# Optimization experiments

Measured on AMD Instinct MI355X. Metric: run time of the kernel, lower is better.

## Reference

```python
import jax, jax.numpy as jnp
import numpy as np

FEATURE_DIM = 512
HIDDEN_DIM = 512
N_HEADS = 8
HEAD_DIM = HIDDEN_DIM // N_HEADS
MAX_LEN = 5000
GAMMA = 0.5  # gaussian relative-position bias width
LN_EPS = 1e-5


def make_pe(d_model, max_len):
    # sinusoidal positional encoding buffer, as in PositionalEncoding.__init__
    pos = jnp.arange(max_len, dtype=jnp.float32)[:, None]
    div = jnp.exp(jnp.arange(0, d_model, 2, dtype=jnp.float32) * (-np.log(10000.0) / d_model))
    ang = pos * div  # [max_len, d_model/2]
    pe = jnp.zeros((max_len, d_model), dtype=jnp.float32)
    pe = pe.at[:, 0::2].set(jnp.sin(ang)).at[:, 1::2].set(jnp.cos(ang))
    return pe


def setup_inputs() -> dict:
    key = jax.random.key(0)
    k_x, k_q, k_k, k_v = jax.random.split(key, 4)
    xavier = np.sqrt(6.0 / (FEATURE_DIM + HEAD_DIM))  # xavier_uniform over last two dims
    return {
        "data_window": jax.random.normal(k_x, (1, 2048, FEATURE_DIM), dtype=jnp.float32),
        "W_query": jax.random.uniform(k_q, (N_HEADS, FEATURE_DIM, HEAD_DIM), jnp.float32, -xavier, xavier),
        "W_key": jax.random.uniform(k_k, (N_HEADS, FEATURE_DIM, HEAD_DIM), jnp.float32, -xavier, xavier),
        "W_value": jax.random.uniform(k_v, (N_HEADS, FEATURE_DIM, HEAD_DIM), jnp.float32, -xavier, xavier),
        "ln_gamma": jnp.ones((FEATURE_DIM,), dtype=jnp.float32),
        "ln_beta": jnp.zeros((FEATURE_DIM,), dtype=jnp.float32),
    }


def reference(data_window, W_query, W_key, W_value, ln_gamma, ln_beta):
    B, S, F = data_window.shape
    temperature = 1.0

    # LayerNorm over feature dim
    mu = jnp.mean(data_window, axis=-1, keepdims=True)
    var = jnp.mean(jnp.square(data_window - mu), axis=-1, keepdims=True)
    x = (data_window - mu) * jax.lax.rsqrt(var + LN_EPS) * ln_gamma + ln_beta

    # positional encoding, exactly as original: x + pe[:x.shape[0]] (requires B==1)
    pe = make_pe(FEATURE_DIM, MAX_LEN)
    x = x + pe[:B]  # [B,F] broadcasts over [B,S,F] only because B==1

    # per-head QKV projections, vectorized over heads
    Q = jnp.einsum('bsf,hfd->bhsd', x, W_query)
    K = jnp.einsum('bsf,hfd->bhsd', x, W_key)
    V = jnp.einsum('bsf,hfd->bhsd', x, W_value)

    scores = jnp.einsum('bhsd,bhtd->bhst', Q, K) / np.sqrt(HEAD_DIM)

    # gaussian relative-position bias: scale(=1) * exp(-gamma * (i-j)^2)
    p = jnp.arange(S, dtype=jnp.float32)
    rel = p[:, None] - p[None, :]
    bias = jnp.exp(-GAMMA * jnp.square(rel))  # [S,S]
    scores = (scores + bias[None, None]) / temperature
    # dropout on scores is identity in eval mode

    attn = jax.nn.softmax(scores, axis=-1)  # [B,H,S,S]
    head_out = jnp.einsum('bhst,bhtd->bhsd', attn, V)

    # concat heads along feature dim: [B,S,H*D]
    multi_head_output = head_out.transpose(0, 2, 1, 3).reshape(B, S, N_HEADS * HEAD_DIM)
    mean_weights = jnp.mean(attn, axis=1)  # [B,S,S]
    return multi_head_output, mean_weights
```

## Files before the change

### kernel.cpp

```cpp
#include <hip/hip_runtime.h>
#include <hip/hip_bf16.h>
#include <math.h>

#define S_LEN 2048
#define FDIM  512
#define NH    8
#define HD    64
#define MH_ELEMS (S_LEN * FDIM)
#define MEAN_ELEMS (S_LEN * S_LEN)
#define LOG2E 1.44269504f
#define LN2   0.69314718f

typedef _Float16 half_t;
typedef _Float16 half2v __attribute__((ext_vector_type(2)));
typedef _Float16 half4v __attribute__((ext_vector_type(4)));
typedef _Float16 half8v __attribute__((ext_vector_type(8)));
typedef float    float4v __attribute__((ext_vector_type(4)));
typedef int      int4v   __attribute__((ext_vector_type(4)));

#define MFMA16(a, b, c) __builtin_amdgcn_mfma_f32_16x16x32_f16((a), (b), (c), 0, 0, 0)

static __device__ __forceinline__ float fast_exp2(float x) {
    return __builtin_amdgcn_exp2f(x);
}

__global__ __launch_bounds__(256) void prep_kernel(const float* __restrict__ x,
                                                   const float* __restrict__ gamma,
                                                   const float* __restrict__ beta,
                                                   const float* __restrict__ Wq,
                                                   const float* __restrict__ Wk,
                                                   const float* __restrict__ Wv,
                                                   half_t* __restrict__ xo,
                                                   half_t* __restrict__ WT) {
    const int tid = threadIdx.x;
    if (blockIdx.x < 2048) {
        const int row = blockIdx.x;
        const float2 v = ((const float2*)(x + (size_t)row * FDIM))[tid];
        float s = v.x + v.y;
        float q = v.x * v.x + v.y * v.y;
        #pragma unroll
        for (int off = 1; off < 64; off <<= 1) {
            s += __shfl_xor(s, off, 64);
            q += __shfl_xor(q, off, 64);
        }
        __shared__ float red[8];
        const int wave = tid >> 6;
        if ((tid & 63) == 0) { red[wave] = s; red[4 + wave] = q; }
        __syncthreads();
        s = red[0] + red[1] + red[2] + red[3];
        q = red[4] + red[5] + red[6] + red[7];
        const float mu  = s * (1.0f / FDIM);
        const float var = q * (1.0f / FDIM) - mu * mu;
        const float rstd = rsqrtf(var + 1e-5f);
        const int f0 = tid * 2, f1 = tid * 2 + 1;
        const float o0 = (v.x - mu) * rstd * gamma[f0] + beta[f0];
        const float o1 = (v.y - mu) * rstd * gamma[f1] + beta[f1] + 1.0f;
        half2v o; o.x = (half_t)o0; o.y = (half_t)o1;
        ((half2v*)(xo + (size_t)row * FDIM))[tid] = o;
    } else {
        const int idx = blockIdx.x - 2048;
        const int k0 = (idx & 7) * 64;
        const int h  = (idx >> 3) & 7;
        const int z  = idx >> 6;
        const float* W = ((z == 0) ? Wq : (z == 1) ? Wk : Wv) + (size_t)h * FDIM * HD;
        __shared__ float Ls[64][65];
        {
            const int kk = tid >> 2, dg = (tid & 3) * 16;
            #pragma unroll
            for (int j = 0; j < 4; ++j) {
                const float4 w = *(const float4*)(W + (size_t)(k0 + kk) * HD + dg + j * 4);
                Ls[kk][dg + j * 4 + 0] = w.x; Ls[kk][dg + j * 4 + 1] = w.y;
                Ls[kk][dg + j * 4 + 2] = w.z; Ls[kk][dg + j * 4 + 3] = w.w;
            }
        }
        __syncthreads();
        {
            const int d = tid >> 2, kg = (tid & 3) * 16;
            half8v t0, t1;
            #pragma unroll
            for (int j = 0; j < 8; ++j) t0[j] = (half_t)Ls[kg + j][d];
            #pragma unroll
            for (int j = 0; j < 8; ++j) t1[j] = (half_t)Ls[kg + 8 + j][d];
            half_t* dst = WT + ((size_t)(z * NH + h) * HD + d) * FDIM + k0 + kg;
            *(half8v*)dst = t0;
            *(half8v*)(dst + 8) = t1;
        }
    }
}

__global__ __launch_bounds__(256) void qkv_kernel(const half_t* __restrict__ xh,
                                                  const half_t* __restrict__ WT,
                                                  half_t* __restrict__ Qo,
                                                  half_t* __restrict__ Ko,
                                                  half_t* __restrict__ VTo) {
    const int ms0 = blockIdx.x * 128;
    const int h   = blockIdx.y, z = blockIdx.z;
    const half_t* Wt = WT + (size_t)(z * NH + h) * HD * FDIM;

    const int tid = threadIdx.x;
    const int wv = tid >> 6, lane = tid & 63;
    const int lo = lane & 15, qq = lane >> 4;

    float4v acc[2][4];
    #pragma unroll
    for (int rg = 0; rg < 2; ++rg)
        #pragma unroll
        for (int cg = 0; cg < 4; ++cg) acc[rg][cg] = (float4v){0.f, 0.f, 0.f, 0.f};

    const half_t* ar[2];
    ar[0] = xh + (size_t)(ms0 + wv * 32 + lo) * FDIM + qq * 8;
    ar[1] = ar[0] + 16 * FDIM;
    const half_t* wrow[4];
    #pragma unroll
    for (int cg = 0; cg < 4; ++cg) wrow[cg] = Wt + (size_t)(cg * 16 + lo) * FDIM + qq * 8;

    half8v a_c[2][2], b_c[4][2];
    #pragma unroll
    for (int rg = 0; rg < 2; ++rg) { a_c[rg][0] = *(const half8v*)(ar[rg]); a_c[rg][1] = *(const half8v*)(ar[rg] + 32); }
    #pragma unroll
    for (int cg = 0; cg < 4; ++cg) { b_c[cg][0] = *(const half8v*)(wrow[cg]); b_c[cg][1] = *(const half8v*)(wrow[cg] + 32); }

    for (int k0 = 0; k0 < FDIM; k0 += 64) {
        const int kn0 = (k0 + 64 < FDIM) ? k0 + 64 : 0;
        const int kn1 = (k0 + 96 < FDIM) ? k0 + 96 : 0;
        half8v a_n[2][2], b_n[4][2];
        #pragma unroll
        for (int rg = 0; rg < 2; ++rg) { a_n[rg][0] = *(const half8v*)(ar[rg] + kn0); a_n[rg][1] = *(const half8v*)(ar[rg] + kn1); }
        #pragma unroll
        for (int cg = 0; cg < 4; ++cg) { b_n[cg][0] = *(const half8v*)(wrow[cg] + kn0); b_n[cg][1] = *(const half8v*)(wrow[cg] + kn1); }
        #pragma unroll
        for (int kh = 0; kh < 2; ++kh)
            #pragma unroll
            for (int rg = 0; rg < 2; ++rg)
                #pragma unroll
                for (int cg = 0; cg < 4; ++cg)
                    acc[rg][cg] = MFMA16(a_c[rg][kh], b_c[cg][kh], acc[rg][cg]);
        #pragma unroll
        for (int rg = 0; rg < 2; ++rg) { a_c[rg][0] = a_n[rg][0]; a_c[rg][1] = a_n[rg][1]; }
        #pragma unroll
        for (int cg = 0; cg < 4; ++cg) { b_c[cg][0] = b_n[cg][0]; b_c[cg][1] = b_n[cg][1]; }
    }

    if (z < 2) {
        half_t* Co = ((z == 0) ? Qo : Ko) + (size_t)h * S_LEN * HD;
        #pragma unroll
        for (int rg = 0; rg < 2; ++rg)
            #pragma unroll
            for (int cg = 0; cg < 4; ++cg)
                #pragma unroll
                for (int r = 0; r < 4; ++r)
                    Co[(size_t)(ms0 + wv * 32 + rg * 16 + qq * 4 + r) * HD + cg * 16 + lo] =
                        (half_t)acc[rg][cg][r];
    } else {
        __shared__ float Ls[128][65];
        #pragma unroll
        for (int rg = 0; rg < 2; ++rg)
            #pragma unroll
            for (int cg = 0; cg < 4; ++cg)
                #pragma unroll
                for (int r = 0; r < 4; ++r)
                    Ls[wv * 32 + rg * 16 + qq * 4 + r][cg * 16 + lo] = acc[rg][cg][r];
        __syncthreads();
        const int d = tid & 63, sg = tid >> 6;
        half_t* dst = VTo + (size_t)(h * HD + d) * S_LEN + ms0 + sg * 32;
        #pragma unroll
        for (int c = 0; c < 4; ++c) {
            half8v t;
            #pragma unroll
            for (int j = 0; j < 8; ++j) t[j] = (half_t)Ls[sg * 32 + c * 8 + j][d];
            *(half8v*)(dst + c * 8) = t;
        }
    }
}

__global__ __launch_bounds__(256) void attn2_kernel(const half_t* __restrict__ Qw,
                                                    const half_t* __restrict__ Kw,
                                                    const half_t* __restrict__ VT,
                                                    half_t* __restrict__ Op,
                                                    float* __restrict__ mp,
                                                    float* __restrict__ lp) {
    const int s0 = blockIdx.x * 32;
    const int h  = blockIdx.y;
    const int z  = blockIdx.z;
    const half_t* Qh = Qw + (size_t)h * S_LEN * HD;
    const half_t* Kh = Kw + (size_t)h * S_LEN * HD;
    const half_t* Vt = VT + (size_t)h * (size_t)HD * S_LEN;

    __shared__ float Osh[4][32][65];
    __shared__ float lsh[4][32];
    __shared__ float msh[4][32];

    const int tid = threadIdx.x;
    const int wv = tid >> 6, lane = tid & 63;
    const int lo = lane & 15, qq = lane >> 4;
    const int tb = z * 1024 + wv * 256;

    const half8v qA0 = *(const half8v*)(Qh + (size_t)(s0 + lo) * HD + qq * 8);
    const half8v qA1 = *(const half8v*)(Qh + (size_t)(s0 + lo) * HD + 32 + qq * 8);
    const half8v qB0 = *(const half8v*)(Qh + (size_t)(s0 + 16 + lo) * HD + qq * 8);
    const half8v qB1 = *(const half8v*)(Qh + (size_t)(s0 + 16 + lo) * HD + 32 + qq * 8);

    float4v accA[4], accB[4];
    #pragma unroll
    for (int dt = 0; dt < 4; ++dt) {
        accA[dt] = (float4v){0.f, 0.f, 0.f, 0.f};
        accB[dt] = (float4v){0.f, 0.f, 0.f, 0.f};
    }
    float mA = 0.f, mB = 0.f, lA = 0.f, lB = 0.f;

    const int srcLow  = lo + ((qq & 1) * 2) * 16;
    const int srcHigh = srcLow + 16;
    const bool sel1 = (qq >> 1) != 0;

    half8v kc[4];
    {
        const half_t* kp0 = Kh + (size_t)(tb + lo) * HD;
        const half_t* kp1 = Kh + (size_t)(tb + 16 + lo) * HD;
        kc[0] = *(const half8v*)(kp0 + qq * 8);
        kc[1] = *(const half8v*)(kp0 + 32 + qq * 8);
        kc[2] = *(const half8v*)(kp1 + qq * 8);
        kc[3] = *(const half8v*)(kp1 + 32 + qq * 8);
    }

    for (int ps = 0; ps < 8; ++ps) {
        const int Tg  = tb + ps * 32;
        const int Tgn = tb + ((ps < 7) ? ps + 1 : ps) * 32;
        half8v kn[4], vc[4];
        {
            const half_t* kp0 = Kh + (size_t)(Tgn + lo) * HD;
            const half_t* kp1 = Kh + (size_t)(Tgn + 16 + lo) * HD;
            kn[0] = *(const half8v*)(kp0 + qq * 8);
            kn[1] = *(const half8v*)(kp0 + 32 + qq * 8);
            kn[2] = *(const half8v*)(kp1 + qq * 8);
            kn[3] = *(const half8v*)(kp1 + 32 + qq * 8);
            #pragma unroll
            for (int dt = 0; dt < 4; ++dt)
                vc[dt] = *(const half8v*)(Vt + (size_t)(dt * 16 + lo) * S_LEN + Tg + qq * 8);
        }
        float4v c0A = (float4v){0.f, 0.f, 0.f, 0.f};
        c0A = MFMA16(kc[0], qA0, c0A); c0A = MFMA16(kc[1], qA1, c0A);
        float4v c1A = (float4v){0.f, 0.f, 0.f, 0.f};
        c1A = MFMA16(kc[2], qA0, c1A); c1A = MFMA16(kc[3], qA1, c1A);
        float4v c0B = (float4v){0.f, 0.f, 0.f, 0.f};
        c0B = MFMA16(kc[0], qB0, c0B); c0B = MFMA16(kc[1], qB1, c0B);
        float4v c1B = (float4v){0.f, 0.f, 0.f, 0.f};
        c1B = MFMA16(kc[2], qB0, c1B); c1B = MFMA16(kc[3], qB1, c1B);

        const int dd0 = s0 - Tg;
        const bool nA0 = (dd0 > -40) && (dd0 < 40);
        const bool nA1 = (dd0 - 16 > -40) && (dd0 - 16 < 40);
        const bool nB0 = (dd0 + 16 > -40) && (dd0 + 16 < 40);
        const bool nB1 = nA0;
        float S0A[4], S1A[4], S0B[4], S1B[4];
        #pragma unroll
        for (int r = 0; r < 4; ++r) {
            const int t0 = Tg + qq * 4 + r, t1 = t0 + 16;
            float sa0 = c0A[r] * 0.125f;
            if (nA0) { const float d = (float)(s0 + lo - t0); sa0 += __expf(-0.5f * d * d); }
            float sa1 = c1A[r] * 0.125f;
            if (nA1) { const float d = (float)(s0 + lo - t1); sa1 += __expf(-0.5f * d * d); }
            float sb0 = c0B[r] * 0.125f;
            if (nB0) { const float d = (float)(s0 + 16 + lo - t0); sb0 += __expf(-0.5f * d * d); }
            float sb1 = c1B[r] * 0.125f;
            if (nB1) { const float d = (float)(s0 + 16 + lo - t1); sb1 += __expf(-0.5f * d * d); }
            S0A[r] = sa0 * LOG2E; S1A[r] = sa1 * LOG2E;
            S0B[r] = sb0 * LOG2E; S1B[r] = sb1 * LOG2E;
        }
        float smA = fmaxf(fmaxf(fmaxf(S0A[0], S0A[1]), fmaxf(S0A[2], S0A[3])),
                          fmaxf(fmaxf(S1A[0], S1A[1]), fmaxf(S1A[2], S1A[3])));
        float smB = fmaxf(fmaxf(fmaxf(S0B[0], S0B[1]), fmaxf(S0B[2], S0B[3])),
                          fmaxf(fmaxf(S1B[0], S1B[1]), fmaxf(S1B[2], S1B[3])));
        smA = fmaxf(smA, __shfl_xor(smA, 16, 64));
        smA = fmaxf(smA, __shfl_xor(smA, 32, 64));
        smB = fmaxf(smB, __shfl_xor(smB, 16, 64));
        smB = fmaxf(smB, __shfl_xor(smB, 32, 64));
        const float gmax = fmaxf(smA - mA, smB - mB);
        if (!__all(gmax <= 5.77f)) {
            const float mnA = fmaxf(mA, smA), mnB = fmaxf(mB, smB);
            const float alA = fast_exp2(mA - mnA), alB = fast_exp2(mB - mnB);
            mA = mnA; mB = mnB;
            lA *= alA; lB *= alB;
            #pragma unroll
            for (int dt = 0; dt < 4; ++dt)
                #pragma unroll
                for (int i = 0; i < 4; ++i) { accA[dt][i] *= alA; accB[dt][i] *= alB; }
        }
        float E0A[4], E1A[4], E0B[4], E1B[4];
        float lsA = 0.f, lsB = 0.f;
        #pragma unroll
        for (int r = 0; r < 4; ++r) {
            E0A[r] = fast_exp2(S0A[r] - mA); E1A[r] = fast_exp2(S1A[r] - mA);
            E0B[r] = fast_exp2(S0B[r] - mB); E1B[r] = fast_exp2(S1B[r] - mB);
            lsA += E0A[r] + E1A[r];
            lsB += E0B[r] + E1B[r];
        }
        lA += lsA;
        lB += lsB;

        int pkA0, pkA1, pkA2, pkA3, pkB0, pkB1, pkB2, pkB3;
        {
            half2v p;
            p.x = (half_t)E0A[0]; p.y = (half_t)E0A[1]; pkA0 = __builtin_bit_cast(int, p);
            p.x = (half_t)E0A[2]; p.y = (half_t)E0A[3]; pkA1 = __builtin_bit_cast(int, p);
            p.x = (half_t)E1A[0]; p.y = (half_t)E1A[1]; pkA2 = __builtin_bit_cast(int, p);
            p.x = (half_t)E1A[2]; p.y = (half_t)E1A[3]; pkA3 = __builtin_bit_cast(int, p);
            p.x = (half_t)E0B[0]; p.y = (half_t)E0B[1]; pkB0 = __builtin_bit_cast(int, p);
            p.x = (half_t)E0B[2]; p.y = (half_t)E0B[3]; pkB1 = __builtin_bit_cast(int, p);
            p.x = (half_t)E1B[0]; p.y = (half_t)E1B[1]; pkB2 = __builtin_bit_cast(int, p);
            p.x = (half_t)E1B[2]; p.y = (half_t)E1B[3]; pkB3 = __builtin_bit_cast(int, p);
        }
        int4v biA, biB;
        {
            const int l0a = __shfl(pkA0, srcLow, 64),  l0b = __shfl(pkA2, srcLow, 64);
            const int l1a = __shfl(pkA1, srcLow, 64),  l1b = __shfl(pkA3, srcLow, 64);
            const int h0a = __shfl(pkA0, srcHigh, 64), h0b = __shfl(pkA2, srcHigh, 64);
            const int h1a = __shfl(pkA1, srcHigh, 64), h1b = __shfl(pkA3, srcHigh, 64);
            biA[0] = sel1 ? l0b : l0a;
            biA[1] = sel1 ? l1b : l1a;
            biA[2] = sel1 ? h0b : h0a;
            biA[3] = sel1 ? h1b : h1a;
        }
        {
            const int l0a = __shfl(pkB0, srcLow, 64),  l0b = __shfl(pkB2, srcLow, 64);
            const int l1a = __shfl(pkB1, srcLow, 64),  l1b = __shfl(pkB3, srcLow, 64);
            const int h0a = __shfl(pkB0, srcHigh, 64), h0b = __shfl(pkB2, srcHigh, 64);
            const int h1a = __shfl(pkB1, srcHigh, 64), h1b = __shfl(pkB3, srcHigh, 64);
            biB[0] = sel1 ? l0b : l0a;
            biB[1] = sel1 ? l1b : l1a;
            biB[2] = sel1 ? h0b : h0a;
            biB[3] = sel1 ? h1b : h1a;
        }
        const half8v bpA = __builtin_bit_cast(half8v, biA);
        const half8v bpB = __builtin_bit_cast(half8v, biB);
        #pragma unroll
        for (int dt = 0; dt < 4; ++dt) {
            accA[dt] = MFMA16(vc[dt], bpA, accA[dt]);
            accB[dt] = MFMA16(vc[dt], bpB, accB[dt]);
        }
        #pragma unroll
        for (int i = 0; i < 4; ++i) kc[i] = kn[i];
    }

    lA += __shfl_xor(lA, 16, 64); lA += __shfl_xor(lA, 32, 64);
    lB += __shfl_xor(lB, 16, 64); lB += __shfl_xor(lB, 32, 64);
    if (qq == 0) {
        lsh[wv][lo] = lA;      msh[wv][lo] = mA;
        lsh[wv][16 + lo] = lB; msh[wv][16 + lo] = mB;
    }
    #pragma unroll
    for (int dt = 0; dt < 4; ++dt)
        #pragma unroll
        for (int r = 0; r < 4; ++r) {
            Osh[wv][lo][dt * 16 + qq * 4 + r]      = accA[dt][r];
            Osh[wv][16 + lo][dt * 16 + qq * 4 + r] = accB[dt][r];
        }
    __syncthreads();

    #pragma unroll
    for (int p = 0; p < 2; ++p) {
        const int q = p * 16 + (tid >> 4), dg = tid & 15;
        const float m0 = msh[0][q], m1 = msh[1][q], m2 = msh[2][q], m3 = msh[3][q];
        const float M = fmaxf(fmaxf(m0, m1), fmaxf(m2, m3));
        const float f0 = fast_exp2(m0 - M), f1 = fast_exp2(m1 - M);
        const float f2 = fast_exp2(m2 - M), f3 = fast_exp2(m3 - M);
        const float L = lsh[0][q] * f0 + lsh[1][q] * f1 + lsh[2][q] * f2 + lsh[3][q] * f3;
        half4v o;
        #pragma unroll
        for (int i = 0; i < 4; ++i) {
            const float ov = Osh[0][q][dg * 4 + i] * f0 + Osh[1][q][dg * 4 + i] * f1 +
                             Osh[2][q][dg * 4 + i] * f2 + Osh[3][q][dg * 4 + i] * f3;
            o[i] = (half_t)ov;
        }
        const size_t pidx = (size_t)(z * NH + h) * S_LEN + s0 + q;
        *(half4v*)(Op + pidx * HD + dg * 4) = o;
        if (dg == 0) { mp[pidx] = M * LN2; lp[pidx] = L; }
    }
}

__global__ __launch_bounds__(256) void mean2_kernel(const half_t* __restrict__ Qw,
                                                    const half_t* __restrict__ Kw,
                                                    const half_t* __restrict__ Op,
                                                    const float* __restrict__ mp,
                                                    const float* __restrict__ lp,
                                                    float* __restrict__ out) {
    const int q0 = blockIdx.x * 32;
    const int tbase = blockIdx.y * 256;
    const int tid = threadIdx.x;

    __shared__ float lnc[NH][32];
    __shared__ float g0s[NH][32];
    __shared__ float g1s[NH][32];
    {
        const int h = tid >> 5, qi = tid & 31;
        const size_t i0 = (size_t)h * S_LEN + q0 + qi;
        const size_t i1 = (size_t)(NH + h) * S_LEN + q0 + qi;
        const float m0 = mp[i0], m1 = mp[i1];
        const float M = fmaxf(m0, m1);
        const float f0 = __expf(m0 - M), f1 = __expf(m1 - M);
        const float L = lp[i0] * f0 + lp[i1] * f1;
        const float inv = 1.0f / L;
        lnc[h][qi] = -M - __logf(L);
        g0s[h][qi] = f0 * inv;
        g1s[h][qi] = f1 * inv;
    }
    __syncthreads();

    const int wv = tid >> 6, lane = tid & 63;
    const int lo = lane & 15, qq = lane >> 4;
    const int t0 = tbase + wv * 64;

    float4v macc[2][4];
    #pragma unroll
    for (int rg = 0; rg < 2; ++rg)
        #pragma unroll
        for (int tg = 0; tg < 4; ++tg) macc[rg][tg] = (float4v){0.f, 0.f, 0.f, 0.f};

    const half_t* qp = Qw + (size_t)(q0 + lo) * HD + qq * 8;
    const half_t* kp = Kw + (size_t)(t0 + lo) * HD + qq * 8;

    #pragma unroll 2
    for (int h = 0; h < NH; ++h) {
        half8v a[2][2], b[4][2];
        #pragma unroll
        for (int rg = 0; rg < 2; ++rg) {
            a[rg][0] = *(const half8v*)(qp + (size_t)rg * 16 * HD);
            a[rg][1] = *(const half8v*)(qp + (size_t)rg * 16 * HD + 32);
        }
        #pragma unroll
        for (int tg = 0; tg < 4; ++tg) {
            b[tg][0] = *(const half8v*)(kp + (size_t)tg * 16 * HD);
            b[tg][1] = *(const half8v*)(kp + (size_t)tg * 16 * HD + 32);
        }
        float4v sacc[2][4];
        #pragma unroll
        for (int rg = 0; rg < 2; ++rg)
            #pragma unroll
            for (int tg = 0; tg < 4; ++tg) sacc[rg][tg] = (float4v){0.f, 0.f, 0.f, 0.f};
        #pragma unroll
        for (int kh = 0; kh < 2; ++kh)
            #pragma unroll
            for (int rg = 0; rg < 2; ++rg)
                #pragma unroll
                for (int tg = 0; tg < 4; ++tg)
                    sacc[rg][tg] = MFMA16(a[rg][kh], b[tg][kh], sacc[rg][tg]);

        const float4v ln0 = *(const float4v*)&lnc[h][qq * 4];
        const float4v ln1 = *(const float4v*)&lnc[h][16 + qq * 4];
        #pragma unroll
        for (int tg = 0; tg < 4; ++tg)
            #pragma unroll
            for (int r = 0; r < 4; ++r) {
                macc[0][tg][r] += __expf(fmaf(sacc[0][tg][r], 0.125f, ln0[r]));
                macc[1][tg][r] += __expf(fmaf(sacc[1][tg][r], 0.125f, ln1[r]));
            }
        qp += (size_t)S_LEN * HD;
        kp += (size_t)S_LEN * HD;
    }

    #pragma unroll
    for (int rg = 0; rg < 2; ++rg)
        #pragma unroll
        for (int tg = 0; tg < 4; ++tg) {
            const int tgl = t0 + tg * 16;
            const bool near = ((q0 + 31 - tgl) > -40) && ((q0 - (tgl + 15)) < 40);
            #pragma unroll
            for (int r = 0; r < 4; ++r) {
                const int qe = q0 + rg * 16 + qq * 4 + r;
                const int te = tgl + lo;
                float w = macc[rg][tg][r] * 0.125f;
                if (near) {
                    const float d = (float)(qe - te);
                    w *= __expf(__expf(-0.5f * d * d));
                }
                out[MH_ELEMS + (size_t)qe * S_LEN + te] = w;
            }
        }

    if (blockIdx.y == 0) {
        const int qi = tid >> 3, dg = (tid & 7) * 8;
        const int q = q0 + qi;
        #pragma unroll
        for (int h = 0; h < NH; ++h) {
            const half8v o0 = *(const half8v*)(Op + ((size_t)h * S_LEN + q) * HD + dg);
            const half8v o1 = *(const half8v*)(Op + ((size_t)(NH + h) * S_LEN + q) * HD + dg);
            const float a0 = g0s[h][qi], a1 = g1s[h][qi];
            float4 r0, r1;
            r0.x = (float)o0[0] * a0 + (float)o1[0] * a1;
            r0.y = (float)o0[1] * a0 + (float)o1[1] * a1;
            r0.z = (float)o0[2] * a0 + (float)o1[2] * a1;
            r0.w = (float)o0[3] * a0 + (float)o1[3] * a1;
            r1.x = (float)o0[4] * a0 + (float)o1[4] * a1;
            r1.y = (float)o0[5] * a0 + (float)o1[5] * a1;
            r1.z = (float)o0[6] * a0 + (float)o1[6] * a1;
            r1.w = (float)o0[7] * a0 + (float)o1[7] * a1;
            float* dst = out + (size_t)q * FDIM + h * HD + dg;
            *(float4*)dst = r0;
            *(float4*)(dst + 4) = r1;
        }
    }
}

extern "C" void kernel_launch(void* const* d_in, const int* in_sizes, int n_in,
                              void* d_out, int out_size, void* d_ws, size_t ws_size,
                              hipStream_t stream) {
    const float* x  = (const float*)d_in[0];
    const float* Wq = (const float*)d_in[1];
    const float* Wk = (const float*)d_in[2];
    const float* Wv = (const float*)d_in[3];
    const float* g  = (const float*)d_in[4];
    const float* b  = (const float*)d_in[5];
    float* out = (float*)d_out;
    char*  ws  = (char*)d_ws;

    half_t* Qh   = (half_t*)(ws);
    half_t* Kh   = (half_t*)(ws + (2ull  << 20));
    half_t* VT   = (half_t*)(ws + (4ull  << 20));
    half_t* xh   = (half_t*)(ws + (6ull  << 20));
    half_t* WT   = (half_t*)(ws + (8ull  << 20));
    half_t* Op   = (half_t*)(ws + (10ull << 20));
    float*  mp   = (float*) (ws + (14ull << 20));
    float*  lp   = (float*) (ws + (14ull << 20) + (128ull << 10));

    prep_kernel<<<2240, 256, 0, stream>>>(x, g, b, Wq, Wk, Wv, xh, WT);
    qkv_kernel<<<dim3(16, 8, 3), 256, 0, stream>>>(xh, WT, Qh, Kh, VT);
    attn2_kernel<<<dim3(64, 8, 2), 256, 0, stream>>>(Qh, Kh, VT, Op, mp, lp);
    mean2_kernel<<<dim3(64, 8), 256, 0, stream>>>(Qh, Kh, Op, mp, lp, out);
}
```

Before: 161.3 us.

## Shrink QKV tiles, prefetch per-head Q/K in mean kernel, simplify softmax rescaling

The QKV projection kernel now uses 64-row tiles with one row group per wave, doubling the grid to fill more CUs. The mean-weights kernel software-prefetches the next head's Q/K fragments while computing the current head and uses exp2 with a folded log2e scale. The attention kernel drops the lazy rescale threshold and the log2-domain scores, always rescaling accumulators with natural exp. Rescaling every tile adds ALU work in attention, while the other changes aim to hide load latency and improve occupancy.

```diff
diff --git a/kernel.cpp b/kernel.cpp
--- a/kernel.cpp
+++ b/kernel.cpp
@@ -9,7 +9,7 @@
 #define MH_ELEMS (S_LEN * FDIM)
 #define MEAN_ELEMS (S_LEN * S_LEN)
 #define LOG2E 1.44269504f
-#define LN2   0.69314718f
+#define QK_SCALE_L2 0.18033688f
 
 typedef _Float16 half_t;
 typedef _Float16 half2v __attribute__((ext_vector_type(2)));
@@ -93,7 +93,7 @@
                                                   half_t* __restrict__ Qo,
                                                   half_t* __restrict__ Ko,
                                                   half_t* __restrict__ VTo) {
-    const int ms0 = blockIdx.x * 128;
+    const int ms0 = blockIdx.x * 64;
     const int h   = blockIdx.y, z = blockIdx.z;
     const half_t* Wt = WT + (size_t)(z * NH + h) * HD * FDIM;
 
@@ -101,42 +101,33 @@
     const int wv = tid >> 6, lane = tid & 63;
     const int lo = lane & 15, qq = lane >> 4;
 
-    float4v acc[2][4];
-    #pragma unroll
-    for (int rg = 0; rg < 2; ++rg)
-        #pragma unroll
-        for (int cg = 0; cg < 4; ++cg) acc[rg][cg] = (float4v){0.f, 0.f, 0.f, 0.f};
-
-    const half_t* ar[2];
-    ar[0] = xh + (size_t)(ms0 + wv * 32 + lo) * FDIM + qq * 8;
-    ar[1] = ar[0] + 16 * FDIM;
+    float4v acc[4];
+    #pragma unroll
+    for (int cg = 0; cg < 4; ++cg) acc[cg] = (float4v){0.f, 0.f, 0.f, 0.f};
+
+    const half_t* ar = xh + (size_t)(ms0 + wv * 16 + lo) * FDIM + qq * 8;
     const half_t* wrow[4];
     #pragma unroll
     for (int cg = 0; cg < 4; ++cg) wrow[cg] = Wt + (size_t)(cg * 16 + lo) * FDIM + qq * 8;
 
-    half8v a_c[2][2], b_c[4][2];
-    #pragma unroll
-    for (int rg = 0; rg < 2; ++rg) { a_c[rg][0] = *(const half8v*)(ar[rg]); a_c[rg][1] = *(const half8v*)(ar[rg] + 32); }
+    half8v a_c[2], b_c[4][2];
+    a_c[0] = *(const half8v*)(ar); a_c[1] = *(const half8v*)(ar + 32);
     #pragma unroll
     for (int cg = 0; cg < 4; ++cg) { b_c[cg][0] = *(const half8v*)(wrow[cg]); b_c[cg][1] = *(const half8v*)(wrow[cg] + 32); }
 
     for (int k0 = 0; k0 < FDIM; k0 += 64) {
         const int kn0 = (k0 + 64 < FDIM) ? k0 + 64 : 0;
         const int kn1 = (k0 + 96 < FDIM) ? k0 + 96 : 0;
-        half8v a_n[2][2], b_n[4][2];
-        #pragma unroll
-        for (int rg = 0; rg < 2; ++rg) { a_n[rg][0] = *(const half8v*)(ar[rg] + kn0); a_n[rg][1] = *(const half8v*)(ar[rg] + kn1); }
+        half8v a_n[2], b_n[4][2];
+        a_n[0] = *(const half8v*)(ar + kn0); a_n[1] = *(const half8v*)(ar + kn1);
         #pragma unroll
         for (int cg = 0; cg < 4; ++cg) { b_n[cg][0] = *(const half8v*)(wrow[cg] + kn0); b_n[cg][1] = *(const half8v*)(wrow[cg] + kn1); }
         #pragma unroll
         for (int kh = 0; kh < 2; ++kh)
             #pragma unroll
-            for (int rg = 0; rg < 2; ++rg)
-                #pragma unroll
-                for (int cg = 0; cg < 4; ++cg)
-                    acc[rg][cg] = MFMA16(a_c[rg][kh], b_c[cg][kh], acc[rg][cg]);
-        #pragma unroll
-        for (int rg = 0; rg < 2; ++rg) { a_c[rg][0] = a_n[rg][0]; a_c[rg][1] = a_n[rg][1]; }
+            for (int cg = 0; cg < 4; ++cg)
+                acc[cg] = MFMA16(a_c[kh], b_c[cg][kh], acc[cg]);
+        a_c[0] = a_n[0]; a_c[1] = a_n[1];
         #pragma unroll
         for (int cg = 0; cg < 4; ++cg) { b_c[cg][0] = b_n[cg][0]; b_c[cg][1] = b_n[cg][1]; }
     }
@@ -144,30 +135,25 @@
     if (z < 2) {
         half_t* Co = ((z == 0) ? Qo : Ko) + (size_t)h * S_LEN * HD;
         #pragma unroll
-        for (int rg = 0; rg < 2; ++rg)
-            #pragma unroll
-            for (int cg = 0; cg < 4; ++cg)
-                #pragma unroll
-                for (int r = 0; r < 4; ++r)
-                    Co[(size_t)(ms0 + wv * 32 + rg * 16 + qq * 4 + r) * HD + cg * 16 + lo] =
-                        (half_t)acc[rg][cg][r];
+        for (int cg = 0; cg < 4; ++cg)
+            #pragma unroll
+            for (int r = 0; r < 4; ++r)
+                Co[(size_t)(ms0 + wv * 16 + qq * 4 + r) * HD + cg * 16 + lo] = (half_t)acc[cg][r];
     } else {
-        __shared__ float Ls[128][65];
-        #pragma unroll
-        for (int rg = 0; rg < 2; ++rg)
-            #pragma unroll
-            for (int cg = 0; cg < 4; ++cg)
-                #pragma unroll
-                for (int r = 0; r < 4; ++r)
-                    Ls[wv * 32 + rg * 16 + qq * 4 + r][cg * 16 + lo] = acc[rg][cg][r];
+        __shared__ float Ls[64][65];
+        #pragma unroll
+        for (int cg = 0; cg < 4; ++cg)
+            #pragma unroll
+            for (int r = 0; r < 4; ++r)
+                Ls[wv * 16 + qq * 4 + r][cg * 16 + lo] = acc[cg][r];
         __syncthreads();
         const int d = tid & 63, sg = tid >> 6;
-        half_t* dst = VTo + (size_t)(h * HD + d) * S_LEN + ms0 + sg * 32;
-        #pragma unroll
-        for (int c = 0; c < 4; ++c) {
+        half_t* dst = VTo + (size_t)(h * HD + d) * S_LEN + ms0 + sg * 16;
+        #pragma unroll
+        for (int c = 0; c < 2; ++c) {
             half8v t;
             #pragma unroll
-            for (int j = 0; j < 8; ++j) t[j] = (half_t)Ls[sg * 32 + c * 8 + j][d];
+            for (int j = 0; j < 8; ++j) t[j] = (half_t)Ls[sg * 16 + c * 8 + j][d];
             *(half8v*)(dst + c * 8) = t;
         }
     }
@@ -263,8 +249,7 @@
             if (nB0) { const float d = (float)(s0 + 16 + lo - t0); sb0 += __expf(-0.5f * d * d); }
             float sb1 = c1B[r] * 0.125f;
             if (nB1) { const float d = (float)(s0 + 16 + lo - t1); sb1 += __expf(-0.5f * d * d); }
-            S0A[r] = sa0 * LOG2E; S1A[r] = sa1 * LOG2E;
-            S0B[r] = sb0 * LOG2E; S1B[r] = sb1 * LOG2E;
+            S0A[r] = sa0; S1A[r] = sa1; S0B[r] = sb0; S1B[r] = sb1;
         }
         float smA = fmaxf(fmaxf(fmaxf(S0A[0], S0A[1]), fmaxf(S0A[2], S0A[3])),
                           fmaxf(fmaxf(S1A[0], S1A[1]), fmaxf(S1A[2], S1A[3])));
@@ -274,28 +259,24 @@
         smA = fmaxf(smA, __shfl_xor(smA, 32, 64));
         smB = fmaxf(smB, __shfl_xor(smB, 16, 64));
         smB = fmaxf(smB, __shfl_xor(smB, 32, 64));
-        const float gmax = fmaxf(smA - mA, smB - mB);
-        if (!__all(gmax <= 5.77f)) {
-            const float mnA = fmaxf(mA, smA), mnB = fmaxf(mB, smB);
-            const float alA = fast_exp2(mA - mnA), alB = fast_exp2(mB - mnB);
-            mA = mnA; mB = mnB;
-            lA *= alA; lB *= alB;
-            #pragma unroll
-            for (int dt = 0; dt < 4; ++dt)
-                #pragma unroll
-                for (int i = 0; i < 4; ++i) { accA[dt][i] *= alA; accB[dt][i] *= alB; }
-        }
+        const float mnA = fmaxf(mA, smA), mnB = fmaxf(mB, smB);
+        const float alA = __expf(mA - mnA), alB = __expf(mB - mnB);
+        mA = mnA; mB = mnB;
         float E0A[4], E1A[4], E0B[4], E1B[4];
         float lsA = 0.f, lsB = 0.f;
         #pragma unroll
         for (int r = 0; r < 4; ++r) {
-            E0A[r] = fast_exp2(S0A[r] - mA); E1A[r] = fast_exp2(S1A[r] - mA);
-            E0B[r] = fast_exp2(S0B[r] - mB); E1B[r] = fast_exp2(S1B[r] - mB);
+            E0A[r] = __expf(S0A[r] - mnA); E1A[r] = __expf(S1A[r] - mnA);
+            E0B[r] = __expf(S0B[r] - mnB); E1B[r] = __expf(S1B[r] - mnB);
             lsA += E0A[r] + E1A[r];
             lsB += E0B[r] + E1B[r];
         }
-        lA += lsA;
-        lB += lsB;
+        lA = lA * alA + lsA;
+        lB = lB * alB + lsB;
+        #pragma unroll
+        for (int dt = 0; dt < 4; ++dt)
+            #pragma unroll
+            for (int i = 0; i < 4; ++i) { accA[dt][i] *= alA; accB[dt][i] *= alB; }
 
         int pkA0, pkA1, pkA2, pkA3, pkB0, pkB1, pkB2, pkB3;
         {
@@ -361,8 +342,8 @@
         const int q = p * 16 + (tid >> 4), dg = tid & 15;
         const float m0 = msh[0][q], m1 = msh[1][q], m2 = msh[2][q], m3 = msh[3][q];
         const float M = fmaxf(fmaxf(m0, m1), fmaxf(m2, m3));
-        const float f0 = fast_exp2(m0 - M), f1 = fast_exp2(m1 - M);
-        const float f2 = fast_exp2(m2 - M), f3 = fast_exp2(m3 - M);
+        const float f0 = __expf(m0 - M), f1 = __expf(m1 - M);
+        const float f2 = __expf(m2 - M), f3 = __expf(m3 - M);
         const float L = lsh[0][q] * f0 + lsh[1][q] * f1 + lsh[2][q] * f2 + lsh[3][q] * f3;
         half4v o;
         #pragma unroll
@@ -373,7 +354,7 @@
         }
         const size_t pidx = (size_t)(z * NH + h) * S_LEN + s0 + q;
         *(half4v*)(Op + pidx * HD + dg * 4) = o;
-        if (dg == 0) { mp[pidx] = M * LN2; lp[pidx] = L; }
+        if (dg == 0) { mp[pidx] = M; lp[pidx] = L; }
     }
 }
 
@@ -399,7 +380,7 @@
         const float f0 = __expf(m0 - M), f1 = __expf(m1 - M);
         const float L = lp[i0] * f0 + lp[i1] * f1;
         const float inv = 1.0f / L;
-        lnc[h][qi] = -M - __logf(L);
+        lnc[h][qi] = (-M - __logf(L)) * LOG2E;
         g0s[h][qi] = f0 * inv;
         g1s[h][qi] = f1 * inv;
     }
@@ -418,19 +399,36 @@
     const half_t* qp = Qw + (size_t)(q0 + lo) * HD + qq * 8;
     const half_t* kp = Kw + (size_t)(t0 + lo) * HD + qq * 8;
 
-    #pragma unroll 2
+    half8v a_c[2][2], b_c[4][2];
+    #pragma unroll
+    for (int rg = 0; rg < 2; ++rg) {
+        a_c[rg][0] = *(const half8v*)(qp + (size_t)rg * 16 * HD);
+        a_c[rg][1] = *(const half8v*)(qp + (size_t)rg * 16 * HD + 32);
+    }
+    #pragma unroll
+    for (int tg = 0; tg < 4; ++tg) {
+        b_c[tg][0] = *(const half8v*)(kp + (size_t)tg * 16 * HD);
+        b_c[tg][1] = *(const half8v*)(kp + (size_t)tg * 16 * HD + 32);
+    }
+
+    #pragma unroll
     for (int h = 0; h < NH; ++h) {
-        half8v a[2][2], b[4][2];
-        #pragma unroll
-        for (int rg = 0; rg < 2; ++rg) {
-            a[rg][0] = *(const half8v*)(qp + (size_t)rg * 16 * HD);
-            a[rg][1] = *(const half8v*)(qp + (size_t)rg * 16 * HD + 32);
-        }
-        #pragma unroll
-        for (int tg = 0; tg < 4; ++tg) {
-            b[tg][0] = *(const half8v*)(kp + (size_t)tg * 16 * HD);
-            b[tg][1] = *(const half8v*)(kp + (size_t)tg * 16 * HD + 32);
-        }
+        half8v a_n[2][2], b_n[4][2];
+        if (h + 1 < NH) {
+            const half_t* qn = qp + (size_t)S_LEN * HD;
+            const half_t* kn = kp + (size_t)S_LEN * HD;
+            #pragma unroll
+            for (int rg = 0; rg < 2; ++rg) {
+                a_n[rg][0] = *(const half8v*)(qn + (size_t)rg * 16 * HD);
+                a_n[rg][1] = *(const half8v*)(qn + (size_t)rg * 16 * HD + 32);
+            }
+            #pragma unroll
+            for (int tg = 0; tg < 4; ++tg) {
+                b_n[tg][0] = *(const half8v*)(kn + (size_t)tg * 16 * HD);
+                b_n[tg][1] = *(const half8v*)(kn + (size_t)tg * 16 * HD + 32);
+            }
+        }
+
         float4v sacc[2][4];
         #pragma unroll
         for (int rg = 0; rg < 2; ++rg)
@@ -442,7 +440,7 @@
             for (int rg = 0; rg < 2; ++rg)
                 #pragma unroll
                 for (int tg = 0; tg < 4; ++tg)
-                    sacc[rg][tg] = MFMA16(a[rg][kh], b[tg][kh], sacc[rg][tg]);
+                    sacc[rg][tg] = MFMA16(a_c[rg][kh], b_c[tg][kh], sacc[rg][tg]);
 
         const float4v ln0 = *(const float4v*)&lnc[h][qq * 4];
         const float4v ln1 = *(const float4v*)&lnc[h][16 + qq * 4];
@@ -450,11 +448,18 @@
         for (int tg = 0; tg < 4; ++tg)
             #pragma unroll
             for (int r = 0; r < 4; ++r) {
-                macc[0][tg][r] += __expf(fmaf(sacc[0][tg][r], 0.125f, ln0[r]));
-                macc[1][tg][r] += __expf(fmaf(sacc[1][tg][r], 0.125f, ln1[r]));
+                macc[0][tg][r] += fast_exp2(fmaf(sacc[0][tg][r], QK_SCALE_L2, ln0[r]));
+                macc[1][tg][r] += fast_exp2(fmaf(sacc[1][tg][r], QK_SCALE_L2, ln1[r]));
             }
-        qp += (size_t)S_LEN * HD;
-        kp += (size_t)S_LEN * HD;
+
+        if (h + 1 < NH) {
+            #pragma unroll
+            for (int rg = 0; rg < 2; ++rg) { a_c[rg][0] = a_n[rg][0]; a_c[rg][1] = a_n[rg][1]; }
+            #pragma unroll
+            for (int tg = 0; tg < 4; ++tg) { b_c[tg][0] = b_n[tg][0]; b_c[tg][1] = b_n[tg][1]; }
+            qp += (size_t)S_LEN * HD;
+            kp += (size_t)S_LEN * HD;
+        }
     }
 
     #pragma unroll
@@ -522,7 +527,7 @@
     float*  lp   = (float*) (ws + (14ull << 20) + (128ull << 10));
 
     prep_kernel<<<2240, 256, 0, stream>>>(x, g, b, Wq, Wk, Wv, xh, WT);
-    qkv_kernel<<<dim3(16, 8, 3), 256, 0, stream>>>(xh, WT, Qh, Kh, VT);
+    qkv_kernel<<<dim3(32, 8, 3), 256, 0, stream>>>(xh, WT, Qh, Kh, VT);
     attn2_kernel<<<dim3(64, 8, 2), 256, 0, stream>>>(Qh, Kh, VT, Op, mp, lp);
     mean2_kernel<<<dim3(64, 8), 256, 0, stream>>>(Qh, Kh, Op, mp, lp, out);
 }
```

Measured after the change: 168.7 us. +4.6%, slower.
